# Performance work log

Measured on AMD Instinct MI355X. Metric: run time of the kernel, lower is better.

## Reference

```python
import jax, jax.numpy as jnp
import numpy as np

EPS = 1e-8

def div_small(a, b):
    b_safe = b * (b > EPS) + (b <= EPS) * EPS
    return a / b_safe

def cos_full(q1h, q2h, w):
    # q1h [b,s1,h], q2h [b,s1_or_1,h], w [P,h] -> [b,s1,P]
    a = q1h[:, :, None, :] * w          # [b,s1,P,h]
    c = q2h[:, :, None, :] * w          # [b,s1|1,P,h]
    num = jnp.sum(a * c, axis=-1)
    den = jnp.maximum(jnp.linalg.norm(a, axis=-1) * jnp.linalg.norm(c, axis=-1), EPS)
    return num / den

def cos_maxpool(q1h, q2h, w):
    # q1h [b,s1,h], q2h [b,s2,h], w [P,h] -> max over s2 of cosine -> [b,s1,P]
    a = q1h[:, :, None, :] * w          # [b,s1,P,h]
    c = q2h[:, :, None, :] * w          # [b,s2,P,h]
    num = jnp.einsum('biph,bjph->bijp', a, c)            # [b,s1,s2,P]
    na = jnp.linalg.norm(a, axis=-1)                     # [b,s1,P]
    nc = jnp.linalg.norm(c, axis=-1)                     # [b,s2,P]
    den = jnp.maximum(na[:, :, None, :] * nc[:, None, :, :], EPS)
    return jnp.max(num / den, axis=2)

def attention(q1, q2):
    # cosine-similarity matrix [b,s1,s2]
    n1 = jnp.linalg.norm(q1, axis=2, keepdims=True)      # [b,s1,1]
    n2 = jnp.linalg.norm(q2, axis=2, keepdims=True)      # [b,s2,1]
    num = jnp.einsum('bih,bjh->bij', q1, q2)
    return div_small(num, n1 * jnp.swapaxes(n2, 1, 2))

def setup_inputs() -> dict:
    key = jax.random.key(0)
    k1, k2, kw = jax.random.split(key, 3)
    q1_batch = jax.random.normal(k1, (16, 128, 512), dtype=jnp.float32)
    q2_batch = jax.random.normal(k2, (16, 128, 512), dtype=jnp.float32)
    W = jax.random.normal(kw, (8, 16, 256), dtype=jnp.float32)
    return {"q1_batch": q1_batch, "q2_batch": q2_batch, "W": W}

def reference(q1_batch, q2_batch, W):
    h = q1_batch.shape[-1] // 2
    q1_fw, q1_bw = q1_batch[..., :h], q1_batch[..., h:]
    q2_fw, q2_bw = q2_batch[..., :h], q2_batch[..., h:]

    # 1) full matching against last (fw) / first (bw) q2 state
    full_fw = cos_full(q1_fw, q2_fw[:, -1:, :], W[0])
    full_bw = cos_full(q1_bw, q2_bw[:, :1, :], W[1])

    # 2) max-pool matching over all q2 positions
    max_fw = cos_maxpool(q1_fw, q2_fw, W[2])
    max_bw = cos_maxpool(q1_bw, q2_bw, W[3])

    # 3) attentive matching
    att_fw = attention(q1_fw, q2_fw)                     # [b,s1,s2]
    att_bw = attention(q1_bw, q2_bw)
    at_q2_fw = att_fw[..., None] * q2_fw[:, None, :, :]  # [b,s1,s2,h]
    at_q2_bw = att_bw[..., None] * q2_bw[:, None, :, :]
    mean_fw = div_small(at_q2_fw.sum(axis=2), att_fw.sum(axis=2, keepdims=True))
    # NOTE: denominator intentionally uses att_fw (bug preserved from source)
    mean_bw = div_small(at_q2_bw.sum(axis=2), att_fw.sum(axis=2, keepdims=True))
    attn_fw = cos_full(q1_fw, mean_fw, W[4])
    attn_bw = cos_full(q1_bw, mean_bw, W[5])

    # 4) max-attentive matching
    max_at_fw = at_q2_fw.max(axis=2)                     # [b,s1,h]
    max_at_bw = at_q2_bw.max(axis=2)
    maxattn_fw = cos_full(q1_fw, max_at_fw, W[6])
    maxattn_bw = cos_full(q1_bw, max_at_bw, W[7])

    return jnp.concatenate(
        [full_fw, full_bw, max_fw, max_bw, attn_fw, attn_bw, maxattn_fw, maxattn_bw],
        axis=-1)
```

## Files before the change

### kernel.cpp

```cpp
#include <hip/hip_runtime.h>
#include <hip/hip_bf16.h>

#define B 16
#define L 128
#define H 256
#define H2 512
#define P 16
#define EPSF 1e-8f
#define LDSTR 72

typedef __attribute__((ext_vector_type(8))) short short8;
typedef __attribute__((ext_vector_type(4))) short short4v;
typedef __attribute__((ext_vector_type(4))) float f32x4;

__device__ __forceinline__ short f2bf(float x) {
    unsigned u = __builtin_bit_cast(unsigned, x);
    u += 0x7fffu + ((u >> 16) & 1u);
    return (short)(u >> 16);
}
__device__ __forceinline__ float bf2f(short s) {
    unsigned u = ((unsigned)(unsigned short)s) << 16;
    return __builtin_bit_cast(float, u);
}

__global__ void __launch_bounds__(256) k_att_mfma(
        const float* __restrict__ q1, const float* __restrict__ q2,
        float* __restrict__ att_fw, float* __restrict__ att_bw,
        float* __restrict__ attsum) {
    int bd = blockIdx.x;
    int b = bd >> 1, dir = bd & 1;
    int m0 = blockIdx.y * 16;
    int t = threadIdx.x;

    __shared__ short As[16 * LDSTR];
    __shared__ short Bs[128 * LDSTR];
    __shared__ float nA[16], nB[L];
    __shared__ float part[4][16];

    f32x4 acc[2];
    acc[0] = (f32x4){0.f, 0.f, 0.f, 0.f};
    acc[1] = (f32x4){0.f, 0.f, 0.f, 0.f};

    int wave = t >> 6;
    int l = t & 63;
    int q = l >> 4;
    int coll = l & 15;
    int n0 = wave * 32;

    int arow = t >> 4;
    int acol = (t & 15) * 4;
    int brow = t >> 1;
    int bcol0 = (t & 1) * 32;

    const float* q1b = q1 + ((size_t)b * L + m0) * H2 + dir * H;
    const float* q2b = q2 + ((size_t)b * L) * H2 + dir * H;

    float normA = 0.f, normB = 0.f;

    for (int kt = 0; kt < 4; kt++) {
        int k0 = kt * 64;
        {
            float4 va = *(const float4*)(q1b + (size_t)arow * H2 + k0 + acol);
            normA += va.x * va.x + va.y * va.y + va.z * va.z + va.w * va.w;
            short4v sa = { f2bf(va.x), f2bf(va.y), f2bf(va.z), f2bf(va.w) };
            *(short4v*)(As + arow * LDSTR + acol) = sa;
        }
        for (int cc = 0; cc < 8; cc++) {
            float4 vb = *(const float4*)(q2b + (size_t)brow * H2 + k0 + bcol0 + cc * 4);
            normB += vb.x * vb.x + vb.y * vb.y + vb.z * vb.z + vb.w * vb.w;
            short4v sb = { f2bf(vb.x), f2bf(vb.y), f2bf(vb.z), f2bf(vb.w) };
            *(short4v*)(Bs + brow * LDSTR + bcol0 + cc * 4) = sb;
        }
        __syncthreads();
        for (int ks = 0; ks < 2; ks++) {
            int koff = ks * 32 + q * 8;
            short8 af = *(const short8*)(As + coll * LDSTR + koff);
            short8 bf0 = *(const short8*)(Bs + (n0 + coll) * LDSTR + koff);
            short8 bf1 = *(const short8*)(Bs + (n0 + 16 + coll) * LDSTR + koff);
            acc[0] = __builtin_amdgcn_mfma_f32_16x16x32_bf16(af, bf0, acc[0], 0, 0, 0);
            acc[1] = __builtin_amdgcn_mfma_f32_16x16x32_bf16(af, bf1, acc[1], 0, 0, 0);
        }
        __syncthreads();
    }
    {
        float sA = normA;
        for (int off = 1; off < 16; off <<= 1) sA += __shfl_xor(sA, off, 16);
        if ((t & 15) == 0) nA[arow] = sqrtf(sA);
        float sB = normB + __shfl_xor(normB, 1, 2);
        if ((t & 1) == 0) nB[brow] = sqrtf(sB);
    }
    __syncthreads();

    float* attout = dir ? att_bw : att_fw;
    size_t bL = (size_t)b * L;
    float n1v[4];
    for (int r = 0; r < 4; r++) n1v[r] = nA[q * 4 + r];
    float rsum[4] = {0.f, 0.f, 0.f, 0.f};
    for (int nt = 0; nt < 2; nt++) {
        int col = n0 + nt * 16 + coll;
        float n2v = nB[col];
        for (int r = 0; r < 4; r++) {
            int row = m0 + q * 4 + r;
            float den = n1v[r] * n2v;
            den = den > EPSF ? den : EPSF;
            float a = acc[nt][r] / den;
            attout[(bL + row) * L + col] = a;
            rsum[r] += a;
        }
    }
    if (dir == 0) {
        for (int off = 1; off < 16; off <<= 1)
            for (int r = 0; r < 4; r++)
                rsum[r] += __shfl_xor(rsum[r], off, 16);
        if (coll == 0)
            for (int r = 0; r < 4; r++)
                part[wave][q * 4 + r] = rsum[r];
        __syncthreads();
        if (t < 16)
            attsum[bL + m0 + t] = part[0][t] + part[1][t] + part[2][t] + part[3][t];
    }
}

__global__ void __launch_bounds__(256) k_meanmax_v2(
        const float* __restrict__ q2,
        const float* __restrict__ att_fw, const float* __restrict__ att_bw,
        const float* __restrict__ attsum,
        float* __restrict__ mean_fw, float* __restrict__ mean_bw,
        float* __restrict__ maxat_fw, float* __restrict__ maxat_bw) {
    int bd = blockIdx.x;
    int b = bd >> 1, dir = bd & 1;
    int i0 = blockIdx.y * 8;
    int t = threadIdx.x;
    int wave = t >> 6, l = t & 63;

    __shared__ float at[8][L];
    __shared__ float Ss[8];
    __shared__ f32x4 red[4][64][4];

    const float* att = dir ? att_bw : att_fw;
    for (int v = t; v < 8 * L; v += 256) {
        int r = v >> 7, j = v & 127;
        at[r][j] = att[((size_t)b * L + i0 + r) * L + j];
    }
    if (t < 8) {
        float s = attsum[(size_t)b * L + i0 + t];
        Ss[t] = s > EPSF ? s : EPSF;
    }
    __syncthreads();

    f32x4 sum[8], mx[8];
    for (int r = 0; r < 8; r++) {
        sum[r] = (f32x4){0.f, 0.f, 0.f, 0.f};
        mx[r] = (f32x4){-INFINITY, -INFINITY, -INFINITY, -INFINITY};
    }

    const float* q2b = q2 + (size_t)b * L * H2 + dir * H;
    for (int jj = 0; jj < 32; jj++) {
        int j = wave * 32 + jj;
        float4 c = *(const float4*)(q2b + (size_t)j * H2 + l * 4);
        for (int r = 0; r < 8; r++) {
            float w = at[r][j];
            f32x4 v = { w * c.x, w * c.y, w * c.z, w * c.w };
            sum[r] += v;
            mx[r][0] = fmaxf(mx[r][0], v[0]);
            mx[r][1] = fmaxf(mx[r][1], v[1]);
            mx[r][2] = fmaxf(mx[r][2], v[2]);
            mx[r][3] = fmaxf(mx[r][3], v[3]);
        }
    }

    float* meanout = dir ? mean_bw : mean_fw;
    float* maxout = dir ? maxat_bw : maxat_fw;
    for (int rr = 0; rr < 4; rr++) {
        __syncthreads();
        red[wave][l][0] = sum[rr * 2];
        red[wave][l][1] = mx[rr * 2];
        red[wave][l][2] = sum[rr * 2 + 1];
        red[wave][l][3] = mx[rr * 2 + 1];
        __syncthreads();
        if (t < 128) {
            int r2 = t >> 6;
            int lane = t & 63;
            f32x4 s = red[0][lane][r2 * 2];
            f32x4 m = red[0][lane][r2 * 2 + 1];
            for (int w = 1; w < 4; w++) {
                s += red[w][lane][r2 * 2];
                f32x4 m2 = red[w][lane][r2 * 2 + 1];
                m[0] = fmaxf(m[0], m2[0]);
                m[1] = fmaxf(m[1], m2[1]);
                m[2] = fmaxf(m[2], m2[2]);
                m[3] = fmaxf(m[3], m2[3]);
            }
            int row = i0 + rr * 2 + r2;
            float inv = 1.f / Ss[rr * 2 + r2];
            size_t o = ((size_t)b * L + row) * H + lane * 4;
            *(f32x4*)(meanout + o) = s * inv;
            *(f32x4*)(maxout + o) = m;
        }
    }
}

__global__ void __launch_bounds__(256) k_cosfull(
        const float* __restrict__ q1, const float* __restrict__ q2,
        const float* __restrict__ mean_fw, const float* __restrict__ mean_bw,
        const float* __restrict__ maxat_fw, const float* __restrict__ maxat_bw,
        const float* __restrict__ W, float* __restrict__ out) {
    int blk = blockIdx.x;
    int piece = blockIdx.y;
    int b = blk / L;
    int t = threadIdx.x;
    int p = t >> 4, l = t & 15;

    int widx, col, dir;
    const float* vptr;
    switch (piece) {
        case 0: widx = 0; col = 0;   dir = 0; vptr = q2 + ((size_t)b * L + (L - 1)) * H2;  break;
        case 1: widx = 1; col = 16;  dir = 1; vptr = q2 + ((size_t)b * L) * H2 + H;        break;
        case 2: widx = 4; col = 64;  dir = 0; vptr = mean_fw + (size_t)blk * H;            break;
        case 3: widx = 5; col = 80;  dir = 1; vptr = mean_bw + (size_t)blk * H;            break;
        case 4: widx = 6; col = 96;  dir = 0; vptr = maxat_fw + (size_t)blk * H;           break;
        default: widx = 7; col = 112; dir = 1; vptr = maxat_bw + (size_t)blk * H;          break;
    }
    const float* r1 = q1 + (size_t)blk * H2 + dir * H;
    const float* wrow = W + ((size_t)widx * P + p) * H;
    float num = 0, na = 0, nc = 0;
    for (int k = 0; k < 16; k++) {
        int h = l + 16 * k;
        float wv = wrow[h];
        float ws = wv * wv;
        float a = r1[h];
        float c = vptr[h];
        num += a * c * ws;
        na  += a * a * ws;
        nc  += c * c * ws;
    }
    for (int off = 8; off; off >>= 1) {
        num += __shfl_down(num, off, 16);
        na  += __shfl_down(na,  off, 16);
        nc  += __shfl_down(nc,  off, 16);
    }
    if (l == 0) {
        float den = sqrtf(na) * sqrtf(nc);
        den = den > EPSF ? den : EPSF;
        out[(size_t)blk * 128 + col + p] = num / den;
    }
}

__global__ void __launch_bounds__(256, 2) k_maxpool_mfma(
        const float* __restrict__ q1, const float* __restrict__ q2,
        const float* __restrict__ W, float* __restrict__ out) {
    int bd = blockIdx.x;
    int b = bd >> 1, dir = bd & 1;
    int p = blockIdx.y;
    int t = threadIdx.x;

    __shared__ short As[128 * LDSTR];
    __shared__ short Bs[128 * LDSTR];
    __shared__ float wv[H];
    __shared__ float nrm[256];

    wv[t] = W[((size_t)(2 + dir) * P + p) * H + t];
    __syncthreads();

    f32x4 acc[2][8];
    for (int mt = 0; mt < 2; mt++)
        for (int nt = 0; nt < 8; nt++)
            acc[mt][nt] = (f32x4){0.f, 0.f, 0.f, 0.f};

    int lane16 = t & 15;
    int rgrp = t >> 4;
    int nrow = t & 127;
    int nmat = t >> 7;
    float normacc = 0.f;

    int wave = t >> 6;
    int l = t & 63;
    int q = l >> 4;
    int coll = l & 15;
    int m0 = wave * 32;

    const float* q1b = q1 + ((size_t)b * L) * H2 + dir * H;
    const float* q2b = q2 + ((size_t)b * L) * H2 + dir * H;

    for (int kt = 0; kt < 4; kt++) {
        int k0 = kt * 64;
        for (int pass = 0; pass < 8; pass++) {
            int row = rgrp + pass * 16;
            int c4 = lane16 * 4;
            float w0 = wv[k0 + c4], w1 = wv[k0 + c4 + 1];
            float w2 = wv[k0 + c4 + 2], w3 = wv[k0 + c4 + 3];
            float4 va = *(const float4*)(q1b + (size_t)row * H2 + k0 + c4);
            short4v sa = { f2bf(va.x * w0), f2bf(va.y * w1), f2bf(va.z * w2), f2bf(va.w * w3) };
            *(short4v*)(As + row * LDSTR + c4) = sa;
            float4 vb = *(const float4*)(q2b + (size_t)row * H2 + k0 + c4);
            short4v sb = { f2bf(vb.x * w0), f2bf(vb.y * w1), f2bf(vb.z * w2), f2bf(vb.w * w3) };
            *(short4v*)(Bs + row * LDSTR + c4) = sb;
        }
        __syncthreads();
        {
            const short* rowp = (nmat ? Bs : As) + nrow * LDSTR;
            for (int c = 0; c < 8; c++) {
                short8 s = *(const short8*)(rowp + c * 8);
                for (int jj = 0; jj < 8; jj++) {
                    float f = bf2f(s[jj]);
                    normacc += f * f;
                }
            }
        }
        for (int ks = 0; ks < 2; ks++) {
            int koff = ks * 32 + q * 8;
            short8 af0 = *(const short8*)(As + (m0 + coll) * LDSTR + koff);
            short8 af1 = *(const short8*)(As + (m0 + 16 + coll) * LDSTR + koff);
            for (int nt = 0; nt < 8; nt++) {
                short8 bfr = *(const short8*)(Bs + (nt * 16 + coll) * LDSTR + koff);
                acc[0][nt] = __builtin_amdgcn_mfma_f32_16x16x32_bf16(af0, bfr, acc[0][nt], 0, 0, 0);
                acc[1][nt] = __builtin_amdgcn_mfma_f32_16x16x32_bf16(af1, bfr, acc[1][nt], 0, 0, 0);
            }
        }
        __syncthreads();
    }
    nrm[t] = sqrtf(normacc);
    __syncthreads();

    float nav[2][4];
    for (int mt = 0; mt < 2; mt++)
        for (int r = 0; r < 4; r++)
            nav[mt][r] = nrm[m0 + mt * 16 + q * 4 + r];
    float rmax[2][4];
    for (int mt = 0; mt < 2; mt++)
        for (int r = 0; r < 4; r++) rmax[mt][r] = -INFINITY;
    for (int nt = 0; nt < 8; nt++) {
        float ncv = nrm[128 + nt * 16 + coll];
        for (int mt = 0; mt < 2; mt++)
            for (int r = 0; r < 4; r++) {
                float den = fmaxf(nav[mt][r] * ncv, EPSF);
                float v = acc[mt][nt][r] / den;
                rmax[mt][r] = fmaxf(rmax[mt][r], v);
            }
    }
    for (int off = 1; off < 16; off <<= 1)
        for (int mt = 0; mt < 2; mt++)
            for (int r = 0; r < 4; r++)
                rmax[mt][r] = fmaxf(rmax[mt][r], __shfl_xor(rmax[mt][r], off, 16));
    if (coll == 0) {
        for (int mt = 0; mt < 2; mt++)
            for (int r = 0; r < 4; r++) {
                int row = m0 + mt * 16 + q * 4 + r;
                out[((size_t)b * L + row) * 128 + 32 + dir * 16 + p] = rmax[mt][r];
            }
    }
}

extern "C" void kernel_launch(void* const* d_in, const int* in_sizes, int n_in,
                              void* d_out, int out_size, void* d_ws, size_t ws_size,
                              hipStream_t stream) {
    const float* q1 = (const float*)d_in[0];
    const float* q2 = (const float*)d_in[1];
    const float* W  = (const float*)d_in[2];
    float* out = (float*)d_out;

    float* ws = (float*)d_ws;
    float* attsum = ws;
    float* att_fw = attsum + B * L;
    float* att_bw = att_fw + (size_t)B * L * L;
    float* mean_fw = att_bw + (size_t)B * L * L;
    float* mean_bw = mean_fw + (size_t)B * L * H;
    float* maxat_fw = mean_bw + (size_t)B * L * H;
    float* maxat_bw = maxat_fw + (size_t)B * L * H;

    k_att_mfma<<<dim3(B * 2, 8), 256, 0, stream>>>(q1, q2, att_fw, att_bw, attsum);
    k_meanmax_v2<<<dim3(B * 2, 16), 256, 0, stream>>>(q2, att_fw, att_bw, attsum,
                                                      mean_fw, mean_bw, maxat_fw, maxat_bw);
    k_cosfull<<<dim3(B * L, 6), 256, 0, stream>>>(q1, q2, mean_fw, mean_bw,
                                                  maxat_fw, maxat_bw, W, out);
    k_maxpool_mfma<<<dim3(B * 2, P), 256, 0, stream>>>(q1, q2, W, out);
}
```

Measured before the change: 128.7 us.

## Rework all four kernels for finer-grained parallelism and register-direct MFMA operands

The attention kernel becomes a 64-thread block per 16x16 tile that loads operands straight from global memory into MFMA registers. Row sums are accumulated with atomics into a buffer that is zeroed by a memset first. The maxpool kernel splits rows across a third grid dimension and loads the A operand directly, keeping only B in LDS. Meanmax halves the rows handled per block to double the block count. Cosfull processes 8 rows per block and reuses the squared weights held in registers. These changes aim to raise occupancy and cut LDS traffic, at the cost of an extra memset, atomics and redundant norm computation.

```diff
diff --git a/kernel.cpp b/kernel.cpp
--- a/kernel.cpp
+++ b/kernel.cpp
@@ -22,106 +22,76 @@
     unsigned u = ((unsigned)(unsigned short)s) << 16;
     return __builtin_bit_cast(float, u);
 }
-
-__global__ void __launch_bounds__(256) k_att_mfma(
+__device__ __forceinline__ short8 pack8(float4 x, float4 y) {
+    short8 s;
+    s[0] = f2bf(x.x); s[1] = f2bf(x.y); s[2] = f2bf(x.z); s[3] = f2bf(x.w);
+    s[4] = f2bf(y.x); s[5] = f2bf(y.y); s[6] = f2bf(y.z); s[7] = f2bf(y.w);
+    return s;
+}
+__device__ __forceinline__ float dot4(float4 v) {
+    return v.x * v.x + v.y * v.y + v.z * v.z + v.w * v.w;
+}
+__device__ __forceinline__ float4 mul4(float4 a, float4 b) {
+    return make_float4(a.x * b.x, a.y * b.y, a.z * b.z, a.w * b.w);
+}
+
+__global__ void __launch_bounds__(64) k_att_v3(
         const float* __restrict__ q1, const float* __restrict__ q2,
         float* __restrict__ att_fw, float* __restrict__ att_bw,
         float* __restrict__ attsum) {
-    int bd = blockIdx.x;
-    int b = bd >> 1, dir = bd & 1;
-    int m0 = blockIdx.y * 16;
-    int t = threadIdx.x;
-
-    __shared__ short As[16 * LDSTR];
-    __shared__ short Bs[128 * LDSTR];
-    __shared__ float nA[16], nB[L];
-    __shared__ float part[4][16];
-
-    f32x4 acc[2];
-    acc[0] = (f32x4){0.f, 0.f, 0.f, 0.f};
-    acc[1] = (f32x4){0.f, 0.f, 0.f, 0.f};
-
-    int wave = t >> 6;
-    int l = t & 63;
-    int q = l >> 4;
-    int coll = l & 15;
-    int n0 = wave * 32;
-
-    int arow = t >> 4;
-    int acol = (t & 15) * 4;
-    int brow = t >> 1;
-    int bcol0 = (t & 1) * 32;
-
-    const float* q1b = q1 + ((size_t)b * L + m0) * H2 + dir * H;
-    const float* q2b = q2 + ((size_t)b * L) * H2 + dir * H;
-
-    float normA = 0.f, normB = 0.f;
-
-    for (int kt = 0; kt < 4; kt++) {
-        int k0 = kt * 64;
-        {
-            float4 va = *(const float4*)(q1b + (size_t)arow * H2 + k0 + acol);
-            normA += va.x * va.x + va.y * va.y + va.z * va.z + va.w * va.w;
-            short4v sa = { f2bf(va.x), f2bf(va.y), f2bf(va.z), f2bf(va.w) };
-            *(short4v*)(As + arow * LDSTR + acol) = sa;
-        }
-        for (int cc = 0; cc < 8; cc++) {
-            float4 vb = *(const float4*)(q2b + (size_t)brow * H2 + k0 + bcol0 + cc * 4);
-            normB += vb.x * vb.x + vb.y * vb.y + vb.z * vb.z + vb.w * vb.w;
-            short4v sb = { f2bf(vb.x), f2bf(vb.y), f2bf(vb.z), f2bf(vb.w) };
-            *(short4v*)(Bs + brow * LDSTR + bcol0 + cc * 4) = sb;
-        }
-        __syncthreads();
-        for (int ks = 0; ks < 2; ks++) {
-            int koff = ks * 32 + q * 8;
-            short8 af = *(const short8*)(As + coll * LDSTR + koff);
-            short8 bf0 = *(const short8*)(Bs + (n0 + coll) * LDSTR + koff);
-            short8 bf1 = *(const short8*)(Bs + (n0 + 16 + coll) * LDSTR + koff);
-            acc[0] = __builtin_amdgcn_mfma_f32_16x16x32_bf16(af, bf0, acc[0], 0, 0, 0);
-            acc[1] = __builtin_amdgcn_mfma_f32_16x16x32_bf16(af, bf1, acc[1], 0, 0, 0);
-        }
-        __syncthreads();
-    }
-    {
-        float sA = normA;
-        for (int off = 1; off < 16; off <<= 1) sA += __shfl_xor(sA, off, 16);
-        if ((t & 15) == 0) nA[arow] = sqrtf(sA);
-        float sB = normB + __shfl_xor(normB, 1, 2);
-        if ((t & 1) == 0) nB[brow] = sqrtf(sB);
-    }
-    __syncthreads();
+    int bx = blockIdx.x;
+    int b = bx >> 1, dir = bx & 1;
+    int m0 = blockIdx.y * 16, n0 = blockIdx.z * 16;
+    int l = threadIdx.x, q = l >> 4, coll = l & 15;
+    size_t bL = (size_t)b * L;
+
+    const float* arow = q1 + (bL + m0 + coll) * H2 + dir * H;
+    const float* brow = q2 + (bL + n0 + coll) * H2 + dir * H;
+
+    f32x4 acc = (f32x4){0.f, 0.f, 0.f, 0.f};
+    float na = 0.f, nc = 0.f;
+#pragma unroll
+    for (int ks = 0; ks < 8; ks++) {
+        int koff = ks * 32 + q * 8;
+        float4 a0 = *(const float4*)(arow + koff);
+        float4 a1 = *(const float4*)(arow + koff + 4);
+        float4 b0 = *(const float4*)(brow + koff);
+        float4 b1 = *(const float4*)(brow + koff + 4);
+        na += dot4(a0) + dot4(a1);
+        nc += dot4(b0) + dot4(b1);
+        short8 af = pack8(a0, a1);
+        short8 bf = pack8(b0, b1);
+        acc = __builtin_amdgcn_mfma_f32_16x16x32_bf16(af, bf, acc, 0, 0, 0);
+    }
+    na += __shfl_xor(na, 16); na += __shfl_xor(na, 32);
+    nc += __shfl_xor(nc, 16); nc += __shfl_xor(nc, 32);
+    float na_s = sqrtf(na), nc_s = sqrtf(nc);
 
     float* attout = dir ? att_bw : att_fw;
-    size_t bL = (size_t)b * L;
-    float n1v[4];
-    for (int r = 0; r < 4; r++) n1v[r] = nA[q * 4 + r];
-    float rsum[4] = {0.f, 0.f, 0.f, 0.f};
-    for (int nt = 0; nt < 2; nt++) {
-        int col = n0 + nt * 16 + coll;
-        float n2v = nB[col];
-        for (int r = 0; r < 4; r++) {
-            int row = m0 + q * 4 + r;
-            float den = n1v[r] * n2v;
-            den = den > EPSF ? den : EPSF;
-            float a = acc[nt][r] / den;
-            attout[(bL + row) * L + col] = a;
-            rsum[r] += a;
-        }
+    float rsum[4];
+#pragma unroll
+    for (int r = 0; r < 4; r++) {
+        float nar = __shfl(na_s, (l & 48) + q * 4 + r);
+        float den = nar * nc_s;
+        den = den > EPSF ? den : EPSF;
+        float a = acc[r] / den;
+        attout[(bL + m0 + q * 4 + r) * L + n0 + coll] = a;
+        rsum[r] = a;
     }
     if (dir == 0) {
+#pragma unroll
         for (int off = 1; off < 16; off <<= 1)
+#pragma unroll
             for (int r = 0; r < 4; r++)
                 rsum[r] += __shfl_xor(rsum[r], off, 16);
         if (coll == 0)
+#pragma unroll
             for (int r = 0; r < 4; r++)
-                part[wave][q * 4 + r] = rsum[r];
-        __syncthreads();
-        if (t < 16)
-            attsum[bL + m0 + t] = part[0][t] + part[1][t] + part[2][t] + part[3][t];
-    }
-}
-
-__global__ void __launch_bounds__(256) k_meanmax_v2(
+                atomicAdd(&attsum[bL + m0 + q * 4 + r], rsum[r]);
+    }
+}
+
+__global__ void __launch_bounds__(256) k_meanmax_v3(
         const float* __restrict__ q2,
         const float* __restrict__ att_fw, const float* __restrict__ att_bw,
         const float* __restrict__ attsum,
@@ -129,36 +99,36 @@
         float* __restrict__ maxat_fw, float* __restrict__ maxat_bw) {
     int bd = blockIdx.x;
     int b = bd >> 1, dir = bd & 1;
-    int i0 = blockIdx.y * 8;
+    int i0 = blockIdx.y * 4;
     int t = threadIdx.x;
     int wave = t >> 6, l = t & 63;
-
-    __shared__ float at[8][L];
-    __shared__ float Ss[8];
+    size_t bL = (size_t)b * L;
+
+    __shared__ float at[4][L];
+    __shared__ float Ss[4];
     __shared__ f32x4 red[4][64][4];
 
     const float* att = dir ? att_bw : att_fw;
-    for (int v = t; v < 8 * L; v += 256) {
-        int r = v >> 7, j = v & 127;
-        at[r][j] = att[((size_t)b * L + i0 + r) * L + j];
-    }
-    if (t < 8) {
-        float s = attsum[(size_t)b * L + i0 + t];
+    for (int v = t; v < 4 * L; v += 256)
+        at[v >> 7][v & 127] = att[(bL + i0 + (v >> 7)) * L + (v & 127)];
+    if (t < 4) {
+        float s = attsum[bL + i0 + t];
         Ss[t] = s > EPSF ? s : EPSF;
     }
     __syncthreads();
 
-    f32x4 sum[8], mx[8];
-    for (int r = 0; r < 8; r++) {
+    f32x4 sum[4], mx[4];
+#pragma unroll
+    for (int r = 0; r < 4; r++) {
         sum[r] = (f32x4){0.f, 0.f, 0.f, 0.f};
         mx[r] = (f32x4){-INFINITY, -INFINITY, -INFINITY, -INFINITY};
     }
-
-    const float* q2b = q2 + (size_t)b * L * H2 + dir * H;
+    const float* q2b = q2 + bL * H2 + dir * H;
     for (int jj = 0; jj < 32; jj++) {
         int j = wave * 32 + jj;
         float4 c = *(const float4*)(q2b + (size_t)j * H2 + l * 4);
-        for (int r = 0; r < 8; r++) {
+#pragma unroll
+        for (int r = 0; r < 4; r++) {
             float w = at[r][j];
             f32x4 v = { w * c.x, w * c.y, w * c.z, w * c.w };
             sum[r] += v;
@@ -168,10 +138,9 @@
             mx[r][3] = fmaxf(mx[r][3], v[3]);
         }
     }
-
     float* meanout = dir ? mean_bw : mean_fw;
     float* maxout = dir ? maxat_bw : maxat_fw;
-    for (int rr = 0; rr < 4; rr++) {
+    for (int rr = 0; rr < 2; rr++) {
         __syncthreads();
         red[wave][l][0] = sum[rr * 2];
         red[wave][l][1] = mx[rr * 2];
@@ -193,162 +162,167 @@
             }
             int row = i0 + rr * 2 + r2;
             float inv = 1.f / Ss[rr * 2 + r2];
-            size_t o = ((size_t)b * L + row) * H + lane * 4;
+            size_t o = (bL + row) * H + lane * 4;
             *(f32x4*)(meanout + o) = s * inv;
             *(f32x4*)(maxout + o) = m;
         }
     }
 }
 
-__global__ void __launch_bounds__(256) k_cosfull(
+__global__ void __launch_bounds__(256) k_cosfull_v3(
         const float* __restrict__ q1, const float* __restrict__ q2,
         const float* __restrict__ mean_fw, const float* __restrict__ mean_bw,
         const float* __restrict__ maxat_fw, const float* __restrict__ maxat_bw,
         const float* __restrict__ W, float* __restrict__ out) {
-    int blk = blockIdx.x;
+    int bg = blockIdx.x;
+    int b = bg >> 4;
+    int i0 = (bg & 15) * 8;
     int piece = blockIdx.y;
-    int b = blk / L;
     int t = threadIdx.x;
     int p = t >> 4, l = t & 15;
-
-    int widx, col, dir;
-    const float* vptr;
+    size_t bL = (size_t)b * L;
+
+    int widx, colb, dir, cstride;
+    const float* cptr;
     switch (piece) {
-        case 0: widx = 0; col = 0;   dir = 0; vptr = q2 + ((size_t)b * L + (L - 1)) * H2;  break;
-        case 1: widx = 1; col = 16;  dir = 1; vptr = q2 + ((size_t)b * L) * H2 + H;        break;
-        case 2: widx = 4; col = 64;  dir = 0; vptr = mean_fw + (size_t)blk * H;            break;
-        case 3: widx = 5; col = 80;  dir = 1; vptr = mean_bw + (size_t)blk * H;            break;
-        case 4: widx = 6; col = 96;  dir = 0; vptr = maxat_fw + (size_t)blk * H;           break;
-        default: widx = 7; col = 112; dir = 1; vptr = maxat_bw + (size_t)blk * H;          break;
-    }
-    const float* r1 = q1 + (size_t)blk * H2 + dir * H;
+        case 0: widx = 0; colb = 0;   dir = 0; cptr = q2 + (bL + L - 1) * H2;  cstride = 0; break;
+        case 1: widx = 1; colb = 16;  dir = 1; cptr = q2 + bL * H2 + H;        cstride = 0; break;
+        case 2: widx = 4; colb = 64;  dir = 0; cptr = mean_fw + bL * H;        cstride = H; break;
+        case 3: widx = 5; colb = 80;  dir = 1; cptr = mean_bw + bL * H;        cstride = H; break;
+        case 4: widx = 6; colb = 96;  dir = 0; cptr = maxat_fw + bL * H;       cstride = H; break;
+        default: widx = 7; colb = 112; dir = 1; cptr = maxat_bw + bL * H;      cstride = H; break;
+    }
     const float* wrow = W + ((size_t)widx * P + p) * H;
-    float num = 0, na = 0, nc = 0;
+    float wsq[16];
+#pragma unroll
     for (int k = 0; k < 16; k++) {
-        int h = l + 16 * k;
-        float wv = wrow[h];
-        float ws = wv * wv;
-        float a = r1[h];
-        float c = vptr[h];
-        num += a * c * ws;
-        na  += a * a * ws;
-        nc  += c * c * ws;
-    }
-    for (int off = 8; off; off >>= 1) {
-        num += __shfl_down(num, off, 16);
-        na  += __shfl_down(na,  off, 16);
-        nc  += __shfl_down(nc,  off, 16);
-    }
-    if (l == 0) {
-        float den = sqrtf(na) * sqrtf(nc);
-        den = den > EPSF ? den : EPSF;
-        out[(size_t)blk * 128 + col + p] = num / den;
-    }
-}
-
-__global__ void __launch_bounds__(256, 2) k_maxpool_mfma(
+        float wv = wrow[l + 16 * k];
+        wsq[k] = wv * wv;
+    }
+    for (int ii = 0; ii < 8; ii++) {
+        int i = i0 + ii;
+        const float* r1 = q1 + (bL + i) * H2 + dir * H;
+        const float* crow = cptr + (size_t)i * cstride;
+        float num = 0, na = 0, nc = 0;
+#pragma unroll
+        for (int k = 0; k < 16; k++) {
+            int h = l + 16 * k;
+            float a = r1[h];
+            float c = crow[h];
+            num += a * c * wsq[k];
+            na  += a * a * wsq[k];
+            nc  += c * c * wsq[k];
+        }
+        for (int off = 8; off; off >>= 1) {
+            num += __shfl_down(num, off, 16);
+            na  += __shfl_down(na,  off, 16);
+            nc  += __shfl_down(nc,  off, 16);
+        }
+        if (l == 0) {
+            float den = sqrtf(na) * sqrtf(nc);
+            den = den > EPSF ? den : EPSF;
+            out[(bL + i) * 128 + colb + p] = num / den;
+        }
+    }
+}
+
+__global__ void __launch_bounds__(256) k_maxpool_v2(
         const float* __restrict__ q1, const float* __restrict__ q2,
         const float* __restrict__ W, float* __restrict__ out) {
     int bd = blockIdx.x;
     int b = bd >> 1, dir = bd & 1;
     int p = blockIdx.y;
     int t = threadIdx.x;
-
-    __shared__ short As[128 * LDSTR];
+    int wave = t >> 6, l = t & 63;
+    int q = l >> 4, coll = l & 15;
+    int m0 = blockIdx.z * 64 + wave * 16;
+    size_t bL = (size_t)b * L;
+
     __shared__ short Bs[128 * LDSTR];
-    __shared__ float wv[H];
-    __shared__ float nrm[256];
-
-    wv[t] = W[((size_t)(2 + dir) * P + p) * H + t];
+    __shared__ float wf[H];
+    __shared__ float ncs[128];
+
+    if (t < 64)
+        *(float4*)(wf + t * 4) =
+            *(const float4*)(W + ((size_t)(2 + dir) * P + p) * H + t * 4);
     __syncthreads();
 
-    f32x4 acc[2][8];
-    for (int mt = 0; mt < 2; mt++)
-        for (int nt = 0; nt < 8; nt++)
-            acc[mt][nt] = (f32x4){0.f, 0.f, 0.f, 0.f};
-
-    int lane16 = t & 15;
-    int rgrp = t >> 4;
-    int nrow = t & 127;
-    int nmat = t >> 7;
-    float normacc = 0.f;
-
-    int wave = t >> 6;
-    int l = t & 63;
-    int q = l >> 4;
-    int coll = l & 15;
-    int m0 = wave * 32;
-
-    const float* q1b = q1 + ((size_t)b * L) * H2 + dir * H;
-    const float* q2b = q2 + ((size_t)b * L) * H2 + dir * H;
+    f32x4 acc[8];
+#pragma unroll
+    for (int nt = 0; nt < 8; nt++) acc[nt] = (f32x4){0.f, 0.f, 0.f, 0.f};
+    float ncp = 0.f, nap = 0.f;
+
+    int brow = t >> 1, bc0 = (t & 1) * 32;
+    const float* q1b = q1 + bL * H2 + dir * H;
+    const float* q2b = q2 + bL * H2 + dir * H;
+    const float* arow = q1b + (size_t)(m0 + coll) * H2;
+    const float* brp = q2b + (size_t)brow * H2;
 
     for (int kt = 0; kt < 4; kt++) {
         int k0 = kt * 64;
-        for (int pass = 0; pass < 8; pass++) {
-            int row = rgrp + pass * 16;
-            int c4 = lane16 * 4;
-            float w0 = wv[k0 + c4], w1 = wv[k0 + c4 + 1];
-            float w2 = wv[k0 + c4 + 2], w3 = wv[k0 + c4 + 3];
-            float4 va = *(const float4*)(q1b + (size_t)row * H2 + k0 + c4);
-            short4v sa = { f2bf(va.x * w0), f2bf(va.y * w1), f2bf(va.z * w2), f2bf(va.w * w3) };
-            *(short4v*)(As + row * LDSTR + c4) = sa;
-            float4 vb = *(const float4*)(q2b + (size_t)row * H2 + k0 + c4);
-            short4v sb = { f2bf(vb.x * w0), f2bf(vb.y * w1), f2bf(vb.z * w2), f2bf(vb.w * w3) };
-            *(short4v*)(Bs + row * LDSTR + c4) = sb;
+#pragma unroll
+        for (int cc = 0; cc < 8; cc++) {
+            float4 v = *(const float4*)(brp + k0 + bc0 + cc * 4);
+            float4 wv4 = *(const float4*)(wf + k0 + bc0 + cc * 4);
+            float4 x = mul4(v, wv4);
+            short4v s = { f2bf(x.x), f2bf(x.y), f2bf(x.z), f2bf(x.w) };
+            *(short4v*)(Bs + brow * LDSTR + bc0 + cc * 4) = s;
+            float f0 = bf2f(s[0]), f1 = bf2f(s[1]), f2v = bf2f(s[2]), f3 = bf2f(s[3]);
+            ncp += f0 * f0 + f1 * f1 + f2v * f2v + f3 * f3;
         }
         __syncthreads();
-        {
-            const short* rowp = (nmat ? Bs : As) + nrow * LDSTR;
-            for (int c = 0; c < 8; c++) {
-                short8 s = *(const short8*)(rowp + c * 8);
-                for (int jj = 0; jj < 8; jj++) {
-                    float f = bf2f(s[jj]);
-                    normacc += f * f;
-                }
-            }
-        }
+#pragma unroll
         for (int ks = 0; ks < 2; ks++) {
             int koff = ks * 32 + q * 8;
-            short8 af0 = *(const short8*)(As + (m0 + coll) * LDSTR + koff);
-            short8 af1 = *(const short8*)(As + (m0 + 16 + coll) * LDSTR + koff);
+            float4 a0 = *(const float4*)(arow + k0 + koff);
+            float4 a1 = *(const float4*)(arow + k0 + koff + 4);
+            float4 w0 = *(const float4*)(wf + k0 + koff);
+            float4 w1 = *(const float4*)(wf + k0 + koff + 4);
+            float4 e0 = mul4(a0, w0), e1 = mul4(a1, w1);
+            short8 af = pack8(e0, e1);
+#pragma unroll
+            for (int j = 0; j < 8; j++) {
+                float f = bf2f(af[j]);
+                nap += f * f;
+            }
+#pragma unroll
             for (int nt = 0; nt < 8; nt++) {
-                short8 bfr = *(const short8*)(Bs + (nt * 16 + coll) * LDSTR + koff);
-                acc[0][nt] = __builtin_amdgcn_mfma_f32_16x16x32_bf16(af0, bfr, acc[0][nt], 0, 0, 0);
-                acc[1][nt] = __builtin_amdgcn_mfma_f32_16x16x32_bf16(af1, bfr, acc[1][nt], 0, 0, 0);
+                short8 bf = *(const short8*)(Bs + (nt * 16 + coll) * LDSTR + koff);
+                acc[nt] = __builtin_amdgcn_mfma_f32_16x16x32_bf16(af, bf, acc[nt], 0, 0, 0);
             }
         }
         __syncthreads();
     }
-    nrm[t] = sqrtf(normacc);
+    ncp += __shfl_xor(ncp, 1);
+    if ((t & 1) == 0) ncs[brow] = sqrtf(ncp);
+    nap += __shfl_xor(nap, 16);
+    nap += __shfl_xor(nap, 32);
+    float na_s = sqrtf(nap);
     __syncthreads();
 
-    float nav[2][4];
-    for (int mt = 0; mt < 2; mt++)
+    float nar[4];
+#pragma unroll
+    for (int r = 0; r < 4; r++)
+        nar[r] = __shfl(na_s, (l & 48) + q * 4 + r);
+    float rmax[4] = {-INFINITY, -INFINITY, -INFINITY, -INFINITY};
+#pragma unroll
+    for (int nt = 0; nt < 8; nt++) {
+        float ncv = ncs[nt * 16 + coll];
+#pragma unroll
+        for (int r = 0; r < 4; r++) {
+            float den = fmaxf(nar[r] * ncv, EPSF);
+            rmax[r] = fmaxf(rmax[r], acc[nt][r] / den);
+        }
+    }
+#pragma unroll
+    for (int off = 1; off < 16; off <<= 1)
+#pragma unroll
         for (int r = 0; r < 4; r++)
-            nav[mt][r] = nrm[m0 + mt * 16 + q * 4 + r];
-    float rmax[2][4];
-    for (int mt = 0; mt < 2; mt++)
-        for (int r = 0; r < 4; r++) rmax[mt][r] = -INFINITY;
-    for (int nt = 0; nt < 8; nt++) {
-        float ncv = nrm[128 + nt * 16 + coll];
-        for (int mt = 0; mt < 2; mt++)
-            for (int r = 0; r < 4; r++) {
-                float den = fmaxf(nav[mt][r] * ncv, EPSF);
-                float v = acc[mt][nt][r] / den;
-                rmax[mt][r] = fmaxf(rmax[mt][r], v);
-            }
-    }
-    for (int off = 1; off < 16; off <<= 1)
-        for (int mt = 0; mt < 2; mt++)
-            for (int r = 0; r < 4; r++)
-                rmax[mt][r] = fmaxf(rmax[mt][r], __shfl_xor(rmax[mt][r], off, 16));
-    if (coll == 0) {
-        for (int mt = 0; mt < 2; mt++)
-            for (int r = 0; r < 4; r++) {
-                int row = m0 + mt * 16 + q * 4 + r;
-                out[((size_t)b * L + row) * 128 + 32 + dir * 16 + p] = rmax[mt][r];
-            }
-    }
+            rmax[r] = fmaxf(rmax[r], __shfl_xor(rmax[r], off, 16));
+    if (coll == 0)
+#pragma unroll
+        for (int r = 0; r < 4; r++)
+            out[(bL + m0 + q * 4 + r) * 128 + 32 + dir * 16 + p] = rmax[r];
 }
 
 extern "C" void kernel_launch(void* const* d_in, const int* in_sizes, int n_in,
@@ -368,10 +342,11 @@
     float* maxat_fw = mean_bw + (size_t)B * L * H;
     float* maxat_bw = maxat_fw + (size_t)B * L * H;
 
-    k_att_mfma<<<dim3(B * 2, 8), 256, 0, stream>>>(q1, q2, att_fw, att_bw, attsum);
-    k_meanmax_v2<<<dim3(B * 2, 16), 256, 0, stream>>>(q2, att_fw, att_bw, attsum,
+    hipMemsetAsync(attsum, 0, B * L * sizeof(float), stream);
+    k_maxpool_v2<<<dim3(B * 2, P, 2), 256, 0, stream>>>(q1, q2, W, out);
+    k_att_v3<<<dim3(B * 2, 8, 8), 64, 0, stream>>>(q1, q2, att_fw, att_bw, attsum);
+    k_meanmax_v3<<<dim3(B * 2, 32), 256, 0, stream>>>(q2, att_fw, att_bw, attsum,
                                                       mean_fw, mean_bw, maxat_fw, maxat_bw);
-    k_cosfull<<<dim3(B * L, 6), 256, 0, stream>>>(q1, q2, mean_fw, mean_bw,
-                                                  maxat_fw, maxat_bw, W, out);
-    k_maxpool_mfma<<<dim3(B * 2, P), 256, 0, stream>>>(q1, q2, W, out);
-}
+    k_cosfull_v3<<<dim3(B * 16, 6), 256, 0, stream>>>(q1, q2, mean_fw, mean_bw,
+                                                      maxat_fw, maxat_bw, W, out);
+}
```

New measurement: 132.9 us. +3.3%, slower.
